# Kernel tuning notes

Measured on AMD Instinct MI355X. Metric: run time of the kernel, lower is better.

Reference implementation:

```python
import jax, jax.numpy as jnp
import numpy as np

EPS = 1e-8


def _cosine_dist_sim(a, b):
    # rowwise cosine distance/similarity over last dim (matches cosine_distance in source)
    w12 = jnp.sum(a * b, axis=-1)
    w1 = jnp.linalg.norm(a, axis=-1)
    w2 = jnp.linalg.norm(b, axis=-1)
    sim = w12 / (w1 * w2)                      # unclamped, as in source's second return
    dist = 1.0 - w12 / jnp.clip(w1 * w2, EPS)  # clamped, as in source's first return
    return dist, sim


def _hard_negative_ids(anchor, embedding, cand):
    # anchor: [B,D]; embedding: [B,D]; cand: [B,2] candidate negative indices (!= row index)
    ce = embedding[cand]                                   # [B,2,D]
    w12 = jnp.einsum('bd,bkd->bk', anchor, ce)             # [B,2]
    n = jnp.linalg.norm(anchor, axis=-1)[:, None] * jnp.linalg.norm(ce, axis=-1)
    d = 1.0 - w12 / jnp.clip(n, EPS)                       # candidate cosine distances
    return jnp.where(d[:, 1] <= d[:, 0], cand[:, 1], cand[:, 0])  # [B]


def setup_inputs() -> dict:
    B, D = 4096, 1024
    key = jax.random.key(0)
    k1, k2, k3, k4, k5 = jax.random.split(key, 5)
    img = jax.random.normal(k1, (B, D), dtype=jnp.float32)
    txt = jax.random.normal(k2, (B, D), dtype=jnp.float32)
    labels = jnp.arange(B, dtype=jnp.int64) if jax.config.jax_enable_x64 else jnp.arange(B, dtype=jnp.int32)
    locations = jax.random.uniform(k3, (B,), dtype=jnp.float32)
    i = jnp.arange(B)[:, None]
    ci = jax.random.randint(k4, (B, 2), 0, B - 1)
    cand_img = ci + (ci >= i)   # avoid self-index, like ids[ids != i]
    ct = jax.random.randint(k5, (B, 2), 0, B - 1)
    cand_txt = ct + (ct >= i)
    return {"img_embedding": img, "text_embedding": txt, "labels": labels,
            "locations": locations, "cand_img": cand_img, "cand_txt": cand_txt}


def reference(img_embedding, text_embedding, labels, locations, cand_img, cand_txt):
    margin = 0.2  # init kwarg
    # anchors are identity-indexed (anchor_ids = positive_ids = arange(B))
    img_anchor, text_anchor = img_embedding, text_embedding
    # hard negative mining: best of 2 random candidates per row
    image_negative_ids = _hard_negative_ids(text_anchor, img_embedding, cand_img)
    text_negative_ids = _hard_negative_ids(img_anchor, text_embedding, cand_txt)
    text_negative = text_embedding[text_negative_ids]
    img_negative = img_embedding[image_negative_ids]
    # triplet loss, mode='local': relu(pos_dist - neg_dist + margin)
    pos_dist, i2t_cosine = _cosine_dist_sim(img_anchor, text_embedding)
    i2t_neg_dist, _ = _cosine_dist_sim(img_anchor, text_negative)
    t2i_pos_dist, t2i_cosine = _cosine_dist_sim(text_anchor, img_embedding)
    t2i_neg_dist, _ = _cosine_dist_sim(text_anchor, img_negative)
    i2t_triplet = jax.nn.relu(pos_dist - i2t_neg_dist + margin)
    t2i_triplet = jax.nn.relu(t2i_pos_dist - t2i_neg_dist + margin)
    loss = i2t_triplet.mean() + t2i_triplet.mean()
    return loss, i2t_cosine, t2i_cosine
```

## Files before the change

### kernel.cpp

```cpp
#include <hip/hip_runtime.h>


constexpr int B = 4096;
constexpr int D = 1024;
#define EPSF 1e-8f
#define MARGIN 0.2f

__device__ __forceinline__ float waveReduceSum(float v) {
#pragma unroll
    for (int off = 32; off > 0; off >>= 1)
        v += __shfl_xor(v, off, 64);
    return v;
}

__device__ __forceinline__ float dot4(float4 a, float4 b) {
    return a.x * b.x + a.y * b.y + a.z * b.z + a.w * b.w;
}

__global__ __launch_bounds__(256) void fused_rows(
    const float* __restrict__ img, const float* __restrict__ txt,
    const int* __restrict__ ci, const int* __restrict__ ct,
    float* __restrict__ out, float* __restrict__ trip) {
    const int wave = threadIdx.x >> 6;
    const int lane = threadIdx.x & 63;
    const int row = blockIdx.x * 4 + wave;

    const int c0 = ci[row * 2 + 0];
    const int c1 = ci[row * 2 + 1];
    const int e0 = ct[row * 2 + 0];
    const int e1 = ct[row * 2 + 1];

    const float4* __restrict__ ib = (const float4*)(img + (size_t)row * D);
    const float4* __restrict__ tb = (const float4*)(txt + (size_t)row * D);
    const float4* __restrict__ i0 = (const float4*)(img + (size_t)c0 * D);
    const float4* __restrict__ i1 = (const float4*)(img + (size_t)c1 * D);
    const float4* __restrict__ t0 = (const float4*)(txt + (size_t)e0 * D);
    const float4* __restrict__ t1 = (const float4*)(txt + (size_t)e1 * D);

    float sd = 0.f, s1 = 0.f, s2 = 0.f;
    float a0 = 0.f, a1 = 0.f, a2 = 0.f, a3 = 0.f;
    float q0 = 0.f, q1 = 0.f, r0 = 0.f, r1 = 0.f;
#pragma unroll
    for (int j = 0; j < 4; ++j) {
        const int idx = j * 64 + lane;
        float4 A = ib[idx];
        float4 T = tb[idx];
        float4 X0 = i0[idx];
        float4 X1 = i1[idx];
        float4 Y0 = t0[idx];
        float4 Y1 = t1[idx];
        sd += dot4(A, T);
        s1 += dot4(A, A);
        s2 += dot4(T, T);
        a0 += dot4(T, X0);
        q0 += dot4(X0, X0);
        a1 += dot4(T, X1);
        q1 += dot4(X1, X1);
        a2 += dot4(A, Y0);
        r0 += dot4(Y0, Y0);
        a3 += dot4(A, Y1);
        r1 += dot4(Y1, Y1);
    }
    sd = waveReduceSum(sd);
    s1 = waveReduceSum(s1);
    s2 = waveReduceSum(s2);
    a0 = waveReduceSum(a0);
    a1 = waveReduceSum(a1);
    a2 = waveReduceSum(a2);
    a3 = waveReduceSum(a3);
    q0 = waveReduceSum(q0);
    q1 = waveReduceSum(q1);
    r0 = waveReduceSum(r0);
    r1 = waveReduceSum(r1);

    if (lane == 0) {
        const float na = sqrtf(s1);
        const float nb = sqrtf(s2);
        const float prod = na * nb;
        const float cosv = sd / prod;
        const float pos = 1.f - sd / fmaxf(prod, EPSF);
        const float d0 = 1.f - a0 / fmaxf(nb * sqrtf(q0), EPSF);
        const float d1 = 1.f - a1 / fmaxf(nb * sqrtf(q1), EPSF);
        const float t2i_neg = (d1 <= d0) ? d1 : d0;
        const float g0 = 1.f - a2 / fmaxf(na * sqrtf(r0), EPSF);
        const float g1 = 1.f - a3 / fmaxf(na * sqrtf(r1), EPSF);
        const float i2t_neg = (g1 <= g0) ? g1 : g0;

        out[1 + row] = cosv;
        out[1 + B + row] = cosv;
        trip[row] = fmaxf(pos - i2t_neg + MARGIN, 0.f)
                  + fmaxf(pos - t2i_neg + MARGIN, 0.f);
    }
}

__global__ __launch_bounds__(1024) void k_reduce(
    const float* __restrict__ trip, float* __restrict__ out) {
    __shared__ float s[1024];
    const int t = threadIdx.x;
    float v = trip[t] + trip[t + 1024] + trip[t + 2048] + trip[t + 3072];
    s[t] = v;
    __syncthreads();
#pragma unroll
    for (int off = 512; off >= 64; off >>= 1) {
        if (t < off) s[t] += s[t + off];
        __syncthreads();
    }
    if (t < 64) {
        float x = s[t];
        x = waveReduceSum(x);
        if (t == 0) out[0] = x * (1.0f / (float)B);
    }
}

extern "C" void kernel_launch(void* const* d_in, const int* in_sizes, int n_in,
                              void* d_out, int out_size, void* d_ws, size_t ws_size,
                              hipStream_t stream) {
    const float* img = (const float*)d_in[0];
    const float* txt = (const float*)d_in[1];
    const int* ci = (const int*)d_in[4];
    const int* ct = (const int*)d_in[5];
    float* out = (float*)d_out;
    float* trip = (float*)d_ws;

    fused_rows<<<B / 4, 256, 0, stream>>>(img, txt, ci, ct, out, trip);
    k_reduce<<<1, 1024, 0, stream>>>(trip, out);
}
```

Baseline: 93.68 us.

## Process one row per block instead of one row per wave

Changes the work split so each 256-thread block handles a single row, with every thread loading one float4 from each of the six vectors. The wave-level partial sums are then combined through shared memory with a block barrier. The aim is more blocks and more independent loads in flight to saturate memory bandwidth, in exchange for a shared-memory reduction, a __syncthreads per row and four times as many blocks to schedule.

New measurement: 96.08 us. +2.6%, slower.

```diff
diff --git a/kernel.cpp b/kernel.cpp
--- a/kernel.cpp
+++ b/kernel.cpp
@@ -21,69 +21,62 @@
     const float* __restrict__ img, const float* __restrict__ txt,
     const int* __restrict__ ci, const int* __restrict__ ct,
     float* __restrict__ out, float* __restrict__ trip) {
-    const int wave = threadIdx.x >> 6;
-    const int lane = threadIdx.x & 63;
-    const int row = blockIdx.x * 4 + wave;
+    const int row = blockIdx.x;
+    const int t = threadIdx.x;
+    const int wave = t >> 6;
+    const int lane = t & 63;
 
     const int c0 = ci[row * 2 + 0];
     const int c1 = ci[row * 2 + 1];
     const int e0 = ct[row * 2 + 0];
     const int e1 = ct[row * 2 + 1];
 
-    const float4* __restrict__ ib = (const float4*)(img + (size_t)row * D);
-    const float4* __restrict__ tb = (const float4*)(txt + (size_t)row * D);
-    const float4* __restrict__ i0 = (const float4*)(img + (size_t)c0 * D);
-    const float4* __restrict__ i1 = (const float4*)(img + (size_t)c1 * D);
-    const float4* __restrict__ t0 = (const float4*)(txt + (size_t)e0 * D);
-    const float4* __restrict__ t1 = (const float4*)(txt + (size_t)e1 * D);
+    const float4 A  = ((const float4*)(img + (size_t)row * D))[t];
+    const float4 T  = ((const float4*)(txt + (size_t)row * D))[t];
+    const float4 X0 = ((const float4*)(img + (size_t)c0 * D))[t];
+    const float4 X1 = ((const float4*)(img + (size_t)c1 * D))[t];
+    const float4 Y0 = ((const float4*)(txt + (size_t)e0 * D))[t];
+    const float4 Y1 = ((const float4*)(txt + (size_t)e1 * D))[t];
 
-    float sd = 0.f, s1 = 0.f, s2 = 0.f;
-    float a0 = 0.f, a1 = 0.f, a2 = 0.f, a3 = 0.f;
-    float q0 = 0.f, q1 = 0.f, r0 = 0.f, r1 = 0.f;
+    float v[11];
+    v[0] = dot4(A, T);
+    v[1] = dot4(A, A);
+    v[2] = dot4(T, T);
+    v[3] = dot4(T, X0);
+    v[4] = dot4(T, X1);
+    v[5] = dot4(X0, X0);
+    v[6] = dot4(X1, X1);
+    v[7] = dot4(A, Y0);
+    v[8] = dot4(A, Y1);
+    v[9] = dot4(Y0, Y0);
+    v[10] = dot4(Y1, Y1);
+
 #pragma unroll
-    for (int j = 0; j < 4; ++j) {
-        const int idx = j * 64 + lane;
-        float4 A = ib[idx];
-        float4 T = tb[idx];
-        float4 X0 = i0[idx];
-        float4 X1 = i1[idx];
-        float4 Y0 = t0[idx];
-        float4 Y1 = t1[idx];
-        sd += dot4(A, T);
-        s1 += dot4(A, A);
-        s2 += dot4(T, T);
-        a0 += dot4(T, X0);
-        q0 += dot4(X0, X0);
-        a1 += dot4(T, X1);
-        q1 += dot4(X1, X1);
-        a2 += dot4(A, Y0);
-        r0 += dot4(Y0, Y0);
-        a3 += dot4(A, Y1);
-        r1 += dot4(Y1, Y1);
+    for (int i = 0; i < 11; ++i) v[i] = waveReduceSum(v[i]);
+
+    __shared__ float s[4][11];
+    if (lane == 0) {
+#pragma unroll
+        for (int i = 0; i < 11; ++i) s[wave][i] = v[i];
     }
-    sd = waveReduceSum(sd);
-    s1 = waveReduceSum(s1);
-    s2 = waveReduceSum(s2);
-    a0 = waveReduceSum(a0);
-    a1 = waveReduceSum(a1);
-    a2 = waveReduceSum(a2);
-    a3 = waveReduceSum(a3);
-    q0 = waveReduceSum(q0);
-    q1 = waveReduceSum(q1);
-    r0 = waveReduceSum(r0);
-    r1 = waveReduceSum(r1);
+    __syncthreads();
 
-    if (lane == 0) {
-        const float na = sqrtf(s1);
-        const float nb = sqrtf(s2);
+    if (t == 0) {
+        float f[11];
+#pragma unroll
+        for (int i = 0; i < 11; ++i)
+            f[i] = s[0][i] + s[1][i] + s[2][i] + s[3][i];
+
+        const float na = sqrtf(f[1]);
+        const float nb = sqrtf(f[2]);
         const float prod = na * nb;
-        const float cosv = sd / prod;
-        const float pos = 1.f - sd / fmaxf(prod, EPSF);
-        const float d0 = 1.f - a0 / fmaxf(nb * sqrtf(q0), EPSF);
-        const float d1 = 1.f - a1 / fmaxf(nb * sqrtf(q1), EPSF);
+        const float cosv = f[0] / prod;
+        const float pos = 1.f - f[0] / fmaxf(prod, EPSF);
+        const float d0 = 1.f - f[3] / fmaxf(nb * sqrtf(f[5]), EPSF);
+        const float d1 = 1.f - f[4] / fmaxf(nb * sqrtf(f[6]), EPSF);
         const float t2i_neg = (d1 <= d0) ? d1 : d0;
-        const float g0 = 1.f - a2 / fmaxf(na * sqrtf(r0), EPSF);
-        const float g1 = 1.f - a3 / fmaxf(na * sqrtf(r1), EPSF);
+        const float g0 = 1.f - f[7] / fmaxf(na * sqrtf(f[9]), EPSF);
+        const float g1 = 1.f - f[8] / fmaxf(na * sqrtf(f[10]), EPSF);
         const float i2t_neg = (g1 <= g0) ? g1 : g0;
 
         out[1 + row] = cosv;
@@ -122,6 +115,6 @@
     float* out = (float*)d_out;
     float* trip = (float*)d_ws;
 
-    fused_rows<<<B / 4, 256, 0, stream>>>(img, txt, ci, ct, out, trip);
+    fused_rows<<<B, 256, 0, stream>>>(img, txt, ci, ct, out, trip);
     k_reduce<<<1, 1024, 0, stream>>>(trip, out);
 }
```
